# Kernel tuning notes

Hardware: AMD Instinct MI355X
Metric: run time of the kernel (lower is better)

Reference implementation:

```python
import jax, jax.numpy as jnp
import numpy as np

N, T, D, H = 32, 2048, 256, 8


def setup_inputs() -> dict:
    key = jax.random.key(0)
    k1, k2, k3, k4, k5 = jax.random.split(key, 5)
    # xavier-uniform bound for [D,D] and [D,H*D] linears
    b1 = float(np.sqrt(6.0 / (D + D)))
    b2 = float(np.sqrt(6.0 / (H * D + D)))
    return {
        "o_k": jax.random.normal(k1, (N, D), dtype=jnp.float32),
        "memory_key": jax.random.normal(k2, (N, T, D), dtype=jnp.float32),
        "memory_value": jax.random.normal(k3, (N, T, D), dtype=jnp.float32),
        # per-head projection weights, stacked torch Linear weights [H, D_out, D_in]
        "Wm": jax.random.uniform(k4, (H, D, D), jnp.float32, -b1, b1),
        # output projection: torch Linear(H*D -> D): weight [D, H*D], bias [D]
        "Wo_w": jax.random.uniform(k5, (D, H * D), jnp.float32, -b2, b2),
        "Wo_b": jnp.full((D,), 0.01, dtype=jnp.float32),
    }


def reference(o_k, memory_key, memory_value, Wm, Wo_w, Wo_b):
    # per-head projected = tanh(memory_key @ Wm[h].T): [H, N, T, D]
    proj = jnp.tanh(jnp.einsum("ntd,hed->hnte", memory_key, Wm))
    # scores[h,n,t] = proj[h,n,t,:] . o_k[n,:], softmax over T
    scores = jax.nn.softmax(jnp.einsum("hnte,ne->hnt", proj, o_k), axis=-1)
    # weighted sum over T: [H, N, D]
    rep = jnp.einsum("hnt,ntd->hnd", scores, memory_value)
    # concat heads along feature dim (head0 first), then W_o linear
    concat = rep.transpose(1, 0, 2).reshape(N, H * D)
    return concat @ Wo_w.T + Wo_b
```

## Files before the change

kernel.cpp:

```cpp
#include <hip/hip_runtime.h>

#define HH 8
#define NN 32
#define TT 2048
#define DD 256

typedef float f4 __attribute__((ext_vector_type(4)));
typedef float f32x4 __attribute__((ext_vector_type(4)));
typedef _Float16 f16x8 __attribute__((ext_vector_type(8)));
typedef __fp16 fp16x2 __attribute__((ext_vector_type(2)));
typedef unsigned short u16;
typedef u16 u16x8 __attribute__((ext_vector_type(8)));

__device__ __forceinline__ u16 f2h(float x) {
  _Float16 h = (_Float16)x;
  return *(u16*)&h;
}

__device__ __forceinline__ float ftanh(float x) {
  float e = __expf(x + x);
  float r = __builtin_amdgcn_rcpf(e + 1.f);
  return __builtin_fmaf(-2.f, r, 1.f);
}

__device__ __forceinline__ void gl_lds16(const void* g, void* l) {
  __builtin_amdgcn_global_load_lds((const __attribute__((address_space(1))) unsigned*)g,
                                   (__attribute__((address_space(3))) unsigned*)l, 16, 0, 0);
}


__global__ void k_pack(const float* __restrict__ mk, const float* __restrict__ wm,
                       u16* __restrict__ pa, u16* __restrict__ pb) {
  const int bid = blockIdx.x;
  if (bid < 8192) {
    int u = bid * 256 + threadIdx.x;
    int pos  = u & 7;
    int line = (u >> 3) & 63;
    int ks   = (u >> 9) & 7;
    int tb   = (u >> 12) & 15;
    int n    = u >> 16;
    int origpos = pos ^ (line & 7);
    int r   = (line << 1) + (origpos >> 2);
    int ksl = origpos & 3;
    int kb  = (ks << 5) + (ksl << 2);
    const float* src = mk + (((size_t)n * TT + (tb << 7) + r) << 8) + kb;
    f4 v0 = *(const f4*)src;
    f4 v1 = *(const f4*)(src + 16);
    u16 hv[8] = {f2h(v0.x), f2h(v0.y), f2h(v0.z), f2h(v0.w),
                 f2h(v1.x), f2h(v1.y), f2h(v1.z), f2h(v1.w)};
    *(u16x8*)(pa + ((size_t)u << 3)) = *(u16x8*)hv;
  } else {
    int u = (bid - 8192) * 256 + threadIdx.x;
    int pos  = u & 7;
    int line = (u >> 3) & 63;
    int ks   = (u >> 9) & 7;
    int eb   = (u >> 12) & 1;
    int h    = u >> 13;
    int origpos = pos ^ (line & 7);
    int el  = (line << 1) + (origpos >> 2);
    int e   = (eb << 7) + el;
    int ksl = origpos & 3;
    int kb  = (ks << 5) + (ksl << 2);
    const float* src = wm + (((size_t)h * 256 + e) << 8) + kb;
    f4 v0 = *(const f4*)src;
    f4 v1 = *(const f4*)(src + 16);
    u16 hv[8] = {f2h(v0.x), f2h(v0.y), f2h(v0.z), f2h(v0.w),
                 f2h(v1.x), f2h(v1.y), f2h(v1.z), f2h(v1.w)};
    *(u16x8*)(pb + ((size_t)u << 3)) = *(u16x8*)hv;
  }
}

__global__ __launch_bounds__(256, 3) void k_scoresf(
    const float* __restrict__ ok, const u16* __restrict__ pa,
    const u16* __restrict__ pb, float* __restrict__ sc2) {
  __shared__ __align__(1024) u16 lds[3 * 8192];
  __shared__ float red[128][2];

  const int bid = blockIdx.x;
  const int h  = bid & 7;
  const int eb = (bid >> 3) & 1;
  const int tb = (bid >> 4) & 15;
  const int n  = bid >> 8;
  const int tid = threadIdx.x;
  const int wave = tid >> 6;
  const int lane = tid & 63;
  const int wr = wave >> 1, wc = wave & 1;
  const int l15 = lane & 15, lg = lane >> 4;

  int Woff[4], Moff[4];
#pragma unroll
  for (int mi = 0; mi < 4; ++mi) {
    int row = (wr << 6) + (mi << 4) + l15;
    int line = row >> 1;
    int pos = (lg | ((row & 1) << 2)) ^ (line & 7);
    Woff[mi] = 4096 + (line << 6) + (pos << 3);
  }
#pragma unroll
  for (int ni = 0; ni < 4; ++ni) {
    int row = (wc << 6) + (ni << 4) + l15;
    int line = row >> 1;
    int pos = (lg | ((row & 1) << 2)) ^ (line & 7);
    Moff[ni] = (line << 6) + (pos << 3);
  }

  const u16* abase = pa + ((size_t)(n * 16 + tb) << 15);
  const u16* bbase = pb + ((size_t)(h * 2 + eb) << 15);

  f32x4 acc[4][4];
#pragma unroll
  for (int i = 0; i < 4; ++i)
#pragma unroll
    for (int j = 0; j < 4; ++j) acc[i][j] = (f32x4){0.f, 0.f, 0.f, 0.f};

#define STAGE(KS, BUF)                                                          \
  do {                                                                          \
    u16* dst = &lds[(BUF) << 13];                                               \
    _Pragma("unroll") for (int j = 0; j < 4; ++j) {                             \
      const int c = (j << 2) + wave;                                           \
      const u16* src = (j < 2 ? abase + ((KS) << 12) + (c << 9)                 \
                              : bbase + ((KS) << 12) + ((c - 8) << 9)) +        \
                       (lane << 3);                                             \
      gl_lds16(src, dst + (c << 9));                                            \
    }                                                                           \
  } while (0)

#define STEP(BUF, VMC)                                                          \
  do {                                                                          \
    asm volatile("s_waitcnt vmcnt(" #VMC ")" ::: "memory");                     \
    __builtin_amdgcn_s_barrier();                                               \
    __builtin_amdgcn_sched_barrier(0);                                          \
    const u16* buf = &lds[(BUF) << 13];                                         \
    f16x8 wfr[4], mfr[4];                                                       \
    _Pragma("unroll") for (int mi = 0; mi < 4; ++mi)                            \
        wfr[mi] = *(const f16x8*)(buf + Woff[mi]);                              \
    _Pragma("unroll") for (int ni = 0; ni < 4; ++ni)                            \
        mfr[ni] = *(const f16x8*)(buf + Moff[ni]);                              \
    __builtin_amdgcn_s_setprio(1);                                              \
    _Pragma("unroll") for (int mi = 0; mi < 4; ++mi)                            \
        _Pragma("unroll") for (int ni = 0; ni < 4; ++ni)                        \
            acc[mi][ni] = __builtin_amdgcn_mfma_f32_16x16x32_f16(               \
                wfr[mi], mfr[ni], acc[mi][ni], 0, 0, 0);                        \
    __builtin_amdgcn_s_setprio(0);                                              \
    __builtin_amdgcn_sched_barrier(0);                                          \
    __builtin_amdgcn_s_barrier();                                               \
  } while (0)

  STAGE(0, 0);
  STAGE(1, 1);
  STAGE(2, 2); STEP(0, 8);
  STAGE(3, 0); STEP(1, 8);
  STAGE(4, 1); STEP(2, 8);
  STAGE(5, 2); STEP(0, 8);
  STAGE(6, 0); STEP(1, 8);
  STAGE(7, 1); STEP(2, 8);
  STEP(0, 4);
  STEP(1, 0);
#undef STEP
#undef STAGE

#pragma unroll
  for (int mi = 0; mi < 4; ++mi)
#pragma unroll
    for (int ni = 0; ni < 4; ++ni)
#pragma unroll
      for (int j = 0; j < 4; ++j) acc[mi][ni][j] = ftanh(acc[mi][ni][j]);

  union F16x8 { f16x8 v; fp16x2 p[4]; };
  F16x8 a2[2];
#pragma unroll
  for (int q = 0; q < 2; ++q) {
    const float* okb = ok + (n << 8) + (eb << 7) + (wr << 6) + (q << 5) + (lg << 2);
    a2[q].p[0] = __builtin_amdgcn_cvt_pkrtz(okb[0], okb[1]);
    a2[q].p[1] = __builtin_amdgcn_cvt_pkrtz(okb[2], okb[3]);
    a2[q].p[2] = __builtin_amdgcn_cvt_pkrtz(okb[16], okb[17]);
    a2[q].p[3] = __builtin_amdgcn_cvt_pkrtz(okb[18], okb[19]);
  }

  f32x4 d2[4];
#pragma unroll
  for (int ni = 0; ni < 4; ++ni) d2[ni] = (f32x4){0.f, 0.f, 0.f, 0.f};
#pragma unroll
  for (int ni = 0; ni < 4; ++ni) {
#pragma unroll
    for (int q = 0; q < 2; ++q) {
      F16x8 b2;
      b2.p[0] = __builtin_amdgcn_cvt_pkrtz(acc[2 * q][ni][0], acc[2 * q][ni][1]);
      b2.p[1] = __builtin_amdgcn_cvt_pkrtz(acc[2 * q][ni][2], acc[2 * q][ni][3]);
      b2.p[2] = __builtin_amdgcn_cvt_pkrtz(acc[2 * q + 1][ni][0], acc[2 * q + 1][ni][1]);
      b2.p[3] = __builtin_amdgcn_cvt_pkrtz(acc[2 * q + 1][ni][2], acc[2 * q + 1][ni][3]);
      d2[ni] = __builtin_amdgcn_mfma_f32_16x16x32_f16(a2[q].v, b2.v, d2[ni], 0, 0, 0);
    }
  }

  if (lg == 0) {
#pragma unroll
    for (int ni = 0; ni < 4; ++ni)
      red[(wc << 6) + (ni << 4) + l15][wr] = d2[ni][0];
  }
  __syncthreads();
  if (tid < 128) {
    float v = red[tid][0] + red[tid][1];
    sc2[((size_t)((h * 32 + n) * 2 + eb) << 11) + (tb << 7) + tid] = v;
  }
}

__global__ void k_softmax(float* __restrict__ sc2) {
  __shared__ float sm[8];
  const int row = blockIdx.x, tid = threadIdx.x;
  float* b0 = sc2 + ((size_t)row << 12);
  const float* b1 = b0 + 2048;
  f4 a = *(const f4*)(b0 + tid * 8);
  f4 b = *(const f4*)(b0 + tid * 8 + 4);
  f4 a1 = *(const f4*)(b1 + tid * 8);
  f4 b1v = *(const f4*)(b1 + tid * 8 + 4);
  a.x += a1.x; a.y += a1.y; a.z += a1.z; a.w += a1.w;
  b.x += b1v.x; b.y += b1v.y; b.z += b1v.z; b.w += b1v.w;
  float m = fmaxf(fmaxf(fmaxf(a.x, a.y), fmaxf(a.z, a.w)),
                  fmaxf(fmaxf(b.x, b.y), fmaxf(b.z, b.w)));
#pragma unroll
  for (int o = 1; o < 64; o <<= 1) m = fmaxf(m, __shfl_xor(m, o));
  if ((tid & 63) == 0) sm[tid >> 6] = m;
  __syncthreads();
  m = fmaxf(fmaxf(sm[0], sm[1]), fmaxf(sm[2], sm[3]));
  a.x = __expf(a.x - m); a.y = __expf(a.y - m); a.z = __expf(a.z - m); a.w = __expf(a.w - m);
  b.x = __expf(b.x - m); b.y = __expf(b.y - m); b.z = __expf(b.z - m); b.w = __expf(b.w - m);
  float s = a.x + a.y + a.z + a.w + b.x + b.y + b.z + b.w;
#pragma unroll
  for (int o = 1; o < 64; o <<= 1) s += __shfl_xor(s, o);
  if ((tid & 63) == 0) sm[4 + (tid >> 6)] = s;
  __syncthreads();
  s = sm[4] + sm[5] + sm[6] + sm[7];
  float inv = 1.f / s;
  a.x *= inv; a.y *= inv; a.z *= inv; a.w *= inv;
  b.x *= inv; b.y *= inv; b.z *= inv; b.w *= inv;
  *(f4*)(b0 + tid * 8) = a;
  *(f4*)(b0 + tid * 8 + 4) = b;
}

__global__ void k_rep(const float* __restrict__ mv, const float* __restrict__ p,
                      float* __restrict__ rp) {
  __shared__ float pl[8][128];
  __shared__ f4 part[4][64][8];
  const int b = blockIdx.x;
  const int n = b >> 4, sl = b & 15;
  const int tid = threadIdx.x;
  for (int i = tid; i < 1024; i += 256) {
    int h = i >> 7, t = i & 127;
    pl[h][t] = p[(((size_t)h * 32 + n) << 12) + sl * 128 + t];
  }
  __syncthreads();
  const int dq = tid & 63, rr = tid >> 6;
  f4 r[8];
#pragma unroll
  for (int h = 0; h < 8; ++h) r[h] = (f4){0.f, 0.f, 0.f, 0.f};
  const float* src = mv + (((size_t)n * TT + sl * 128 + rr) << 8) + (dq << 2);
#pragma unroll 4
  for (int tt = 0; tt < 32; ++tt) {
    f4 v = *(const f4*)(src + tt * 1024);
    float w0 = 0.f;
#pragma unroll
    for (int h = 0; h < 8; ++h) {
      float pw = pl[h][(tt << 2) + rr];
      r[h].x = fmaf(pw, v.x, r[h].x);
      r[h].y = fmaf(pw, v.y, r[h].y);
      r[h].z = fmaf(pw, v.z, r[h].z);
      r[h].w = fmaf(pw, v.w, r[h].w);
    }
    (void)w0;
  }
#pragma unroll
  for (int h = 0; h < 8; ++h) part[rr][dq][h] = r[h];
  __syncthreads();
#pragma unroll
  for (int pp = 0; pp < 2; ++pp) {
    int q = tid + (pp << 8);
    int hq = q & 7, dqq = q >> 3;
    f4 s = part[0][dqq][hq];
    s.x += part[1][dqq][hq].x + part[2][dqq][hq].x + part[3][dqq][hq].x;
    s.y += part[1][dqq][hq].y + part[2][dqq][hq].y + part[3][dqq][hq].y;
    s.z += part[1][dqq][hq].z + part[2][dqq][hq].z + part[3][dqq][hq].z;
    s.w += part[1][dqq][hq].w + part[2][dqq][hq].w + part[3][dqq][hq].w;
    *(f4*)(rp + (((size_t)n * 16 + sl) << 11) + (hq << 8) + (dqq << 2)) = s;
  }
}

__global__ void k_out(const float* __restrict__ rp, const float* __restrict__ w,
                      const float* __restrict__ bias, float* __restrict__ out) {
  __shared__ float c[2048];
  const int b = blockIdx.x;
  const int n = b >> 3, ic = b & 7;
  const int tid = threadIdx.x;
  for (int j = tid; j < 2048; j += 256) {
    float s = 0.f;
#pragma unroll
    for (int sl = 0; sl < 16; ++sl) s += rp[(((size_t)n * 16 + sl) << 11) + j];
    c[j] = s;
  }
  __syncthreads();
  const int ii = (ic << 5) + (tid >> 3);
  const int seg = tid & 7;
  const f4* wrow = (const f4*)(w + (size_t)ii * 2048 + seg * 256);
  const f4* cc = (const f4*)(c + seg * 256);
  float acc = 0.f;
#pragma unroll 8
  for (int j = 0; j < 64; ++j) {
    f4 wv = wrow[j];
    f4 cv = cc[j];
    acc += wv.x * cv.x + wv.y * cv.y + wv.z * cv.z + wv.w * cv.w;
  }
  acc += __shfl_xor(acc, 1);
  acc += __shfl_xor(acc, 2);
  acc += __shfl_xor(acc, 4);
  if (seg == 0) out[n * 256 + ii] = bias[ii] + acc;
}

extern "C" void kernel_launch(void* const* d_in, const int* in_sizes, int n_in,
                              void* d_out, int out_size, void* d_ws, size_t ws_size,
                              hipStream_t stream) {
  const float* ok  = (const float*)d_in[0];
  const float* mk  = (const float*)d_in[1];
  const float* mv  = (const float*)d_in[2];
  const float* wm  = (const float*)d_in[3];
  const float* wow = (const float*)d_in[4];
  const float* wob = (const float*)d_in[5];
  float* out = (float*)d_out;
  char* ws = (char*)d_ws;

  float* sc2 = (float*)ws;
  u16* pb    = (u16*)(ws + (4u << 20));
  float* rp  = (float*)(ws + (8u << 20));
  u16* pa    = (u16*)(ws + (16u << 20));

  hipLaunchKernelGGL(k_pack,    dim3(8448), dim3(256), 0, stream, mk, wm, pa, pb);
  hipLaunchKernelGGL(k_scoresf, dim3(8192), dim3(256), 0, stream, ok, pa, pb, sc2);
  hipLaunchKernelGGL(k_softmax, dim3(256),  dim3(256), 0, stream, sc2);
  hipLaunchKernelGGL(k_rep,     dim3(512),  dim3(256), 0, stream, mv, sc2, rp);
  hipLaunchKernelGGL(k_out,     dim3(256),  dim3(256), 0, stream, rp, wow, wob, out);
}
```

Baseline: 144.4 us.

## Load MFMA fragments directly from global into registers, remap block order

Removes the LDS staging buffer and barrier-synchronised triple-buffered pipeline in the scores GEMM kernel. Each wave now loads its fp16 fragments straight from the pre-swizzled global layout into registers, using a register rotation (three M buffers, two W buffers) to prefetch ahead of the MFMAs. The block index mapping is also remapped so consecutive blocks share the same memory-key tile for L2 reuse. This drops the LDS footprint and barriers, but each wave re-reads shared tiles from global/L2 and holds more registers.

```diff
diff --git a/kernel.cpp b/kernel.cpp
--- a/kernel.cpp
+++ b/kernel.cpp
@@ -21,11 +21,6 @@
   float e = __expf(x + x);
   float r = __builtin_amdgcn_rcpf(e + 1.f);
   return __builtin_fmaf(-2.f, r, 1.f);
-}
-
-__device__ __forceinline__ void gl_lds16(const void* g, void* l) {
-  __builtin_amdgcn_global_load_lds((const __attribute__((address_space(1))) unsigned*)g,
-                                   (__attribute__((address_space(3))) unsigned*)l, 16, 0, 0);
 }
 
 
@@ -73,14 +68,15 @@
 __global__ __launch_bounds__(256, 3) void k_scoresf(
     const float* __restrict__ ok, const u16* __restrict__ pa,
     const u16* __restrict__ pb, float* __restrict__ sc2) {
-  __shared__ __align__(1024) u16 lds[3 * 8192];
   __shared__ float red[128][2];
 
   const int bid = blockIdx.x;
-  const int h  = bid & 7;
-  const int eb = (bid >> 3) & 1;
-  const int tb = (bid >> 4) & 15;
-  const int n  = bid >> 8;
+  const int r  = (bid & 7) | ((bid >> 7) << 3);
+  const int s  = (bid >> 3) & 15;
+  const int h  = s & 7;
+  const int eb = s >> 3;
+  const int n  = r >> 4;
+  const int tb = r & 15;
   const int tid = threadIdx.x;
   const int wave = tid >> 6;
   const int lane = tid & 63;
@@ -93,7 +89,7 @@
     int row = (wr << 6) + (mi << 4) + l15;
     int line = row >> 1;
     int pos = (lg | ((row & 1) << 2)) ^ (line & 7);
-    Woff[mi] = 4096 + (line << 6) + (pos << 3);
+    Woff[mi] = (line << 6) + (pos << 3);
   }
 #pragma unroll
   for (int ni = 0; ni < 4; ++ni) {
@@ -103,8 +99,8 @@
     Moff[ni] = (line << 6) + (pos << 3);
   }
 
-  const u16* abase = pa + ((size_t)(n * 16 + tb) << 15);
-  const u16* bbase = pb + ((size_t)(h * 2 + eb) << 15);
+  const u16* AB = pa + ((size_t)r << 15);
+  const u16* BB = pb + ((size_t)(h * 2 + eb) << 15);
 
   f32x4 acc[4][4];
 #pragma unroll
@@ -112,51 +108,40 @@
 #pragma unroll
     for (int j = 0; j < 4; ++j) acc[i][j] = (f32x4){0.f, 0.f, 0.f, 0.f};
 
-#define STAGE(KS, BUF)                                                          \
+  f16x8 w0[4], w1[4], m0[4], m1[4], m2[4];
+
+#define LM(BUF, KS)                                                             \
   do {                                                                          \
-    u16* dst = &lds[(BUF) << 13];                                               \
-    _Pragma("unroll") for (int j = 0; j < 4; ++j) {                             \
-      const int c = (j << 2) + wave;                                           \
-      const u16* src = (j < 2 ? abase + ((KS) << 12) + (c << 9)                 \
-                              : bbase + ((KS) << 12) + ((c - 8) << 9)) +        \
-                       (lane << 3);                                             \
-      gl_lds16(src, dst + (c << 9));                                            \
-    }                                                                           \
+    _Pragma("unroll") for (int ni = 0; ni < 4; ++ni)                            \
+        BUF[ni] = *(const f16x8*)(AB + ((KS) << 12) + Moff[ni]);                \
   } while (0)
-
-#define STEP(BUF, VMC)                                                          \
+#define LW(BUF, KS)                                                             \
   do {                                                                          \
-    asm volatile("s_waitcnt vmcnt(" #VMC ")" ::: "memory");                     \
-    __builtin_amdgcn_s_barrier();                                               \
-    __builtin_amdgcn_sched_barrier(0);                                          \
-    const u16* buf = &lds[(BUF) << 13];                                         \
-    f16x8 wfr[4], mfr[4];                                                       \
     _Pragma("unroll") for (int mi = 0; mi < 4; ++mi)                            \
-        wfr[mi] = *(const f16x8*)(buf + Woff[mi]);                              \
-    _Pragma("unroll") for (int ni = 0; ni < 4; ++ni)                            \
-        mfr[ni] = *(const f16x8*)(buf + Moff[ni]);                              \
+        BUF[mi] = *(const f16x8*)(BB + ((KS) << 12) + Woff[mi]);                \
+  } while (0)
+#define MM(WB, MB)                                                              \
+  do {                                                                          \
     __builtin_amdgcn_s_setprio(1);                                              \
     _Pragma("unroll") for (int mi = 0; mi < 4; ++mi)                            \
         _Pragma("unroll") for (int ni = 0; ni < 4; ++ni)                        \
             acc[mi][ni] = __builtin_amdgcn_mfma_f32_16x16x32_f16(               \
-                wfr[mi], mfr[ni], acc[mi][ni], 0, 0, 0);                        \
+                WB[mi], MB[ni], acc[mi][ni], 0, 0, 0);                          \
     __builtin_amdgcn_s_setprio(0);                                              \
-    __builtin_amdgcn_sched_barrier(0);                                          \
-    __builtin_amdgcn_s_barrier();                                               \
   } while (0)
 
-  STAGE(0, 0);
-  STAGE(1, 1);
-  STAGE(2, 2); STEP(0, 8);
-  STAGE(3, 0); STEP(1, 8);
-  STAGE(4, 1); STEP(2, 8);
-  STAGE(5, 2); STEP(0, 8);
-  STAGE(6, 0); STEP(1, 8);
-  STAGE(7, 1); STEP(2, 8);
-  STEP(0, 4);
-  STEP(1, 0);
-#undef STEP
-#undef STAGE
+  LM(m0, 0); LM(m1, 1); LW(w0, 0);
+   LM(m2, 2); LW(w1, 1); __builtin_amdgcn_sched_barrier(0); MM(w0, m0);
+   LM(m0, 3); LW(w0, 2); __builtin_amdgcn_sched_barrier(0); MM(w1, m1);
+   LM(m1, 4); LW(w1, 3); __builtin_amdgcn_sched_barrier(0); MM(w0, m2);
+   LM(m2, 5); LW(w0, 4); __builtin_amdgcn_sched_barrier(0); MM(w1, m0);
+   LM(m0, 6); LW(w1, 5); __builtin_amdgcn_sched_barrier(0); MM(w0, m1);
+   LM(m1, 7); LW(w0, 6); __builtin_amdgcn_sched_barrier(0); MM(w1, m2);
+              LW(w1, 7); __builtin_amdgcn_sched_barrier(0); MM(w0, m0);
+                                                            MM(w1, m1);
+#undef LM
+#undef LW
+#undef MM
 
 #pragma unroll
   for (int mi = 0; mi < 4; ++mi)
@@ -192,6 +177,7 @@
     }
   }
 
+  __syncthreads();
   if (lg == 0) {
 #pragma unroll
     for (int ni = 0; ni < 4; ++ni)
@@ -257,7 +243,6 @@
 #pragma unroll 4
   for (int tt = 0; tt < 32; ++tt) {
     f4 v = *(const f4*)(src + tt * 1024);
-    float w0 = 0.f;
 #pragma unroll
     for (int h = 0; h < 8; ++h) {
       float pw = pl[h][(tt << 2) + rr];
@@ -266,7 +251,6 @@
       r[h].z = fmaf(pw, v.z, r[h].z);
       r[h].w = fmaf(pw, v.w, r[h].w);
     }
-    (void)w0;
   }
 #pragma unroll
   for (int h = 0; h < 8; ++h) part[rr][dq][h] = r[h];
```

Measured after the change: 131.6 us. -8.9%, faster.
